# Performance work log

Hardware: AMD Instinct MI355X
Metric: run time of the kernel (lower is better)

## Reference

```python
import jax, jax.numpy as jnp
import numpy as np

D_IN = 384
HID = 384
D_OUT = 384

def _kaiming(key, fan_in, fan_out):
    return jax.random.normal(key, (fan_in, fan_out), dtype=jnp.float32) * np.sqrt(2.0 / fan_in)

def setup_inputs() -> dict:
    key = jax.random.key(0)
    ks = jax.random.split(key, 12)
    B, O, T = 8, 1024, 8192
    obj_vecs = jax.random.normal(ks[0], (B, O, D_IN), dtype=jnp.float32)
    pred_vecs = jax.random.normal(ks[1], (B, T, D_IN), dtype=jnp.float32)
    edges = jax.random.randint(ks[2], (B, T, 2), 0, O, dtype=jnp.int64)
    # gconv1: [3D -> H -> 2H + Dout]; gconv2: [H -> H -> Dout]
    w1a = _kaiming(ks[3], 3 * D_IN, HID); b1a = jnp.zeros((HID,), jnp.float32)
    w1b = _kaiming(ks[4], HID, 2 * HID + D_OUT); b1b = jnp.zeros((2 * HID + D_OUT,), jnp.float32)
    w2a = _kaiming(ks[5], HID, HID); b2a = jnp.zeros((HID,), jnp.float32)
    w2b = _kaiming(ks[6], HID, D_OUT); b2b = jnp.zeros((D_OUT,), jnp.float32)
    return {"obj_vecs": obj_vecs, "pred_vecs": pred_vecs, "edges": edges,
            "w1a": w1a, "b1a": b1a, "w1b": w1b, "b1b": b1b,
            "w2a": w2a, "b2a": b2a, "w2b": w2b, "b2b": b2b}

def _gconv_forward(obj_vecs, pred_vecs, edges, w1a, b1a, w1b, b1b, w2a, b2a, w2b, b2b):
    B, O, D = obj_vecs.shape
    s_idx = edges[:, :, 0]  # (B, T)
    o_idx = edges[:, :, 1]
    batch = jnp.arange(B)[:, None]
    subj = obj_vecs[batch, s_idx]  # (B, T, D) gather
    objt = obj_vecs[batch, o_idx]
    triple = jnp.concatenate([subj, pred_vecs, objt], axis=-1)  # (B, T, 3D)
    h = jax.nn.relu(triple @ w1a + b1a)
    t = jax.nn.relu(h @ w1b + b1b)  # (B, T, 2H + Dout)
    new_s = t[:, :, :HID]
    new_p = t[:, :, HID:HID + D_OUT]
    new_o = t[:, :, HID + D_OUT:]
    # scatter_add per batch into (O, H) buffers
    def agg(si, oi, vs, vo):
        return jnp.zeros((O, HID), vs.dtype).at[si].add(vs).at[oi].add(vo)
    pooled = jax.vmap(agg)(s_idx, o_idx, new_s, new_o)  # (B, O, H)
    pooled = pooled / jnp.linalg.norm(pooled)  # global Frobenius norm, as in torch .norm()
    out_obj = jax.nn.relu(jax.nn.relu(pooled @ w2a + b2a) @ w2b + b2b)
    return out_obj, new_p

def reference(obj_vecs, pred_vecs, edges, w1a, b1a, w1b, b1b, w2a, b2a, w2b, b2b):
    return _gconv_forward(obj_vecs, pred_vecs, edges, w1a, b1a, w1b, b1b, w2a, b2a, w2b, b2b)
```

## Files before the change

### kernel.cpp

```cpp
#include <hip/hip_runtime.h>
#include <hip/hip_bf16.h>

#define NB 8
#define NT 8192
#define NO 1024
#define DD 384
#define K1 1152
#define M1 65536
#define MO 8192

typedef __attribute__((ext_vector_type(8))) short bf16x8;
typedef __attribute__((ext_vector_type(4))) float f32x4;
typedef __attribute__((ext_vector_type(4))) unsigned short u16x4;

__device__ __forceinline__ unsigned short f2bf(float f) {
    union { float f; unsigned u; } v; v.f = f;
    unsigned r = v.u + 0x7FFFu + ((v.u >> 16) & 1u);
    return (unsigned short)(r >> 16);
}
__device__ __forceinline__ float bf2f(unsigned short h) {
    union { unsigned u; float f; } v; v.u = ((unsigned)h) << 16;
    return v.f;
}
__device__ __forceinline__ bf16x8 pack8(f32x4 a, f32x4 b) {
    bf16x8 r;
    r[0] = (short)f2bf(a[0]); r[1] = (short)f2bf(a[1]);
    r[2] = (short)f2bf(a[2]); r[3] = (short)f2bf(a[3]);
    r[4] = (short)f2bf(b[0]); r[5] = (short)f2bf(b[1]);
    r[6] = (short)f2bf(b[2]); r[7] = (short)f2bf(b[3]);
    return r;
}
__device__ __forceinline__ void gload16(const void* g, void* l) {
    __builtin_amdgcn_global_load_lds(
        (const __attribute__((address_space(1))) unsigned int*)g,
        (__attribute__((address_space(3))) unsigned int*)l, 16, 0, 0);
}

__global__ void k_cvt4(const float* __restrict__ s, unsigned short* __restrict__ d, int n) {
    int i = (blockIdx.x * blockDim.x + threadIdx.x) * 4;
    if (i >= n) return;
    f32x4 v = *(const f32x4*)(s + i);
    u16x4 o;
    o[0] = f2bf(v[0]); o[1] = f2bf(v[1]); o[2] = f2bf(v[2]); o[3] = f2bf(v[3]);
    *(u16x4*)(d + i) = o;
}
__global__ void k_tr(const float* __restrict__ s, unsigned short* __restrict__ d, int K, int N) {
    int k = blockIdx.x;
    int n = blockIdx.y * blockDim.x + threadIdx.x;
    if (n < N) d[n * K + k] = f2bf(s[k * N + n]);
}

__global__ void k_ss1(const float* __restrict__ p, float* __restrict__ partial, int n4) {
    __shared__ float wsum[4];
    int stride = gridDim.x * blockDim.x;
    float s = 0.f;
    for (int i = blockIdx.x * blockDim.x + threadIdx.x; i < n4; i += stride) {
        f32x4 v = *(const f32x4*)(p + i * 4);
        s += v[0] * v[0] + v[1] * v[1] + v[2] * v[2] + v[3] * v[3];
    }
#pragma unroll
    for (int off = 32; off; off >>= 1) s += __shfl_down(s, off, 64);
    if ((threadIdx.x & 63) == 0) wsum[threadIdx.x >> 6] = s;
    __syncthreads();
    if (threadIdx.x == 0)
        partial[blockIdx.x] = wsum[0] + wsum[1] + wsum[2] + wsum[3];
}
__global__ void k_ss2(const float* __restrict__ partial, float* __restrict__ o) {
    float s = partial[threadIdx.x];
#pragma unroll
    for (int off = 32; off; off >>= 1) s += __shfl_down(s, off, 64);
    __shared__ float w0, w1;
    if (threadIdx.x == 0) w0 = s;
    if (threadIdx.x == 64) w1 = s;
    __syncthreads();
    if (threadIdx.x == 0) o[0] = w0 + w1;
}
__global__ void k_normcvt(const float* __restrict__ p, const float* __restrict__ ss,
                          unsigned short* __restrict__ o) {
    int i = (blockIdx.x * blockDim.x + threadIdx.x) * 8;
    float s = rsqrtf(ss[0]);
    f32x4 a = *(const f32x4*)(p + i), b = *(const f32x4*)(p + i + 4);
    a *= s; b *= s;
    *(bf16x8*)(o + i) = pack8(a, b);
}

__global__ void k_hist(const int* __restrict__ edges, int* __restrict__ cnt) {
    int i = blockIdx.x * 256 + threadIdx.x;
    int2 e = *(const int2*)&edges[(size_t)i * 2];
    int b = i >> 13;
    atomicAdd(&cnt[(b << 10) + e.x], 1);
    atomicAdd(&cnt[(b << 10) + e.y], 1);
}
__global__ void k_scan(const int* __restrict__ cnt, int* __restrict__ offs) {
    __shared__ int a[1024];
    int b = blockIdx.x, t = threadIdx.x;
    int own = cnt[(b << 10) + t];
    a[t] = own;
    __syncthreads();
    for (int s = 1; s < 1024; s <<= 1) {
        int v = (t >= s) ? a[t - s] : 0;
        __syncthreads();
        a[t] += v;
        __syncthreads();
    }
    offs[(b << 10) + t] = a[t] - own;
}
__global__ void k_fill(const int* __restrict__ edges, const int* __restrict__ offs,
                       int* __restrict__ cur, int* __restrict__ elist) {
    int i = blockIdx.x * 256 + threadIdx.x;
    int2 e = *(const int2*)&edges[(size_t)i * 2];
    int b = i >> 13, t = i & (NT - 1);
    int ps = atomicAdd(&cur[(b << 10) + e.x], 1);
    elist[(b << 14) + offs[(b << 10) + e.x] + ps] = t * 2;
    int po = atomicAdd(&cur[(b << 10) + e.y], 1);
    elist[(b << 14) + offs[(b << 10) + e.y] + po] = t * 2 + 1;
}
__global__ void k_pool(const unsigned short* __restrict__ sob, const int* __restrict__ cnt,
                       const int* __restrict__ offs, const int* __restrict__ elist,
                       float* __restrict__ pooled) {
    int w = (blockIdx.x * 256 + threadIdx.x) >> 6;
    int lane = threadIdx.x & 63;
    if (lane >= 48) return;
    int b = w >> 10, o = w & (NO - 1);
    int len = cnt[(b << 10) + o];
    const int* lst = elist + (b << 14) + offs[(b << 10) + o];
    f32x4 a0 = {0.f, 0.f, 0.f, 0.f}, a1 = {0.f, 0.f, 0.f, 0.f};
    f32x4 c0 = {0.f, 0.f, 0.f, 0.f}, c1 = {0.f, 0.f, 0.f, 0.f};
    int j = 0;
    for (; j + 1 < len; j += 2) {
        int e0 = lst[j], e1 = lst[j + 1];
        bf16x8 v0 = *(const bf16x8*)(sob + ((size_t)((b << 13) + (e0 >> 1))) * 768 + (e0 & 1) * DD + lane * 8);
        bf16x8 v1 = *(const bf16x8*)(sob + ((size_t)((b << 13) + (e1 >> 1))) * 768 + (e1 & 1) * DD + lane * 8);
        a0[0] += bf2f((unsigned short)v0[0]); a0[1] += bf2f((unsigned short)v0[1]);
        a0[2] += bf2f((unsigned short)v0[2]); a0[3] += bf2f((unsigned short)v0[3]);
        a1[0] += bf2f((unsigned short)v0[4]); a1[1] += bf2f((unsigned short)v0[5]);
        a1[2] += bf2f((unsigned short)v0[6]); a1[3] += bf2f((unsigned short)v0[7]);
        c0[0] += bf2f((unsigned short)v1[0]); c0[1] += bf2f((unsigned short)v1[1]);
        c0[2] += bf2f((unsigned short)v1[2]); c0[3] += bf2f((unsigned short)v1[3]);
        c1[0] += bf2f((unsigned short)v1[4]); c1[1] += bf2f((unsigned short)v1[5]);
        c1[2] += bf2f((unsigned short)v1[6]); c1[3] += bf2f((unsigned short)v1[7]);
    }
    if (j < len) {
        int e0 = lst[j];
        bf16x8 v0 = *(const bf16x8*)(sob + ((size_t)((b << 13) + (e0 >> 1))) * 768 + (e0 & 1) * DD + lane * 8);
        a0[0] += bf2f((unsigned short)v0[0]); a0[1] += bf2f((unsigned short)v0[1]);
        a0[2] += bf2f((unsigned short)v0[2]); a0[3] += bf2f((unsigned short)v0[3]);
        a1[0] += bf2f((unsigned short)v0[4]); a1[1] += bf2f((unsigned short)v0[5]);
        a1[2] += bf2f((unsigned short)v0[6]); a1[3] += bf2f((unsigned short)v0[7]);
    }
    a0 += c0; a1 += c1;
    float* dst = pooled + ((size_t)((b << 10) + o)) * DD + lane * 8;
    *(f32x4*)dst = a0;
    *(f32x4*)(dst + 4) = a1;
}

template <int STAGE, int EPI>
__launch_bounds__(512, 2)
__global__ void gemm_k(const unsigned short* __restrict__ Abf,
                       const unsigned short* __restrict__ objb,
                       const float* __restrict__ predf,
                       const int* __restrict__ edges,
                       const unsigned short* __restrict__ Bt,
                       const float* __restrict__ bias,
                       unsigned short* __restrict__ outb,
                       float* __restrict__ outf,
                       int K, int ldC)
{
    const int tid = threadIdx.x;
    const int lane = tid & 63;
    const int m0 = blockIdx.x * 128;
    const int bt0 = 0;

    __shared__ unsigned short At[128 * 64];
    __shared__ unsigned short Bl[384 * 64];
    __shared__ int eidx[128][2];

    if (STAGE == 1) {
        if (tid < 128) {
            int2 e = *(const int2*)&edges[(size_t)(m0 + tid) * 2];
            eidx[tid][0] = e.x;
            eidx[tid][1] = e.y;
        }
        __syncthreads();
    }

    const int rb = tid >> 3;
    const int c8 = ((tid & 7) ^ (rb & 7)) * 8;

    int er0[2], er1[2];
    if (STAGE == 1) {
        const int bb = (m0 >> 13) << 10;
#pragma unroll
        for (int i = 0; i < 2; ++i) {
            er0[i] = bb + eidx[i * 64 + rb][0];
            er1[i] = bb + eidx[i * 64 + rb][1];
        }
    }

    f32x4 acc[4][6];
#pragma unroll
    for (int i = 0; i < 4; ++i)
#pragma unroll
        for (int j = 0; j < 6; ++j) acc[i][j] = (f32x4){0.f, 0.f, 0.f, 0.f};

    const int wid = tid >> 6, wm = wid >> 2, wn = wid & 3;
    const int l16 = lane & 15, lg = lane >> 4;

    for (int kk = 0; kk < K; kk += 64) {
#pragma unroll
        for (int i = 0; i < 6; ++i)
            gload16(Bt + (size_t)(bt0 + i * 64 + rb) * K + kk + c8, Bl + i * 4096 + tid * 8);
        if (STAGE == 0) {
#pragma unroll
            for (int i = 0; i < 2; ++i)
                gload16(Abf + (size_t)(m0 + i * 64 + rb) * K + kk + c8, At + i * 4096 + tid * 8);
        } else {
            const int seg = kk / DD;
            const int ko = kk - seg * DD;
            if (seg == 1) {
#pragma unroll
                for (int i = 0; i < 2; ++i) {
                    const float* p = predf + (size_t)(m0 + i * 64 + rb) * DD + ko + c8;
                    *(bf16x8*)(At + i * 4096 + tid * 8) = pack8(*(const f32x4*)p, *(const f32x4*)(p + 4));
                }
            } else if (seg == 0) {
#pragma unroll
                for (int i = 0; i < 2; ++i)
                    gload16(objb + (size_t)er0[i] * DD + ko + c8, At + i * 4096 + tid * 8);
            } else {
#pragma unroll
                for (int i = 0; i < 2; ++i)
                    gload16(objb + (size_t)er1[i] * DD + ko + c8, At + i * 4096 + tid * 8);
            }
        }
        __syncthreads();
#pragma unroll
        for (int kt = 0; kt < 2; ++kt) {
            const int cs = ((kt * 4 + lg) ^ (l16 & 7)) * 8;
            bf16x8 af[4], bfr[6];
#pragma unroll
            for (int mt = 0; mt < 4; ++mt)
                af[mt] = *(const bf16x8*)(At + (wm * 64 + mt * 16 + l16) * 64 + cs);
#pragma unroll
            for (int nt = 0; nt < 6; ++nt)
                bfr[nt] = *(const bf16x8*)(Bl + (wn * 96 + nt * 16 + l16) * 64 + cs);
#pragma unroll
            for (int mt = 0; mt < 4; ++mt)
#pragma unroll
                for (int nt = 0; nt < 6; ++nt)
                    acc[mt][nt] = __builtin_amdgcn_mfma_f32_16x16x32_bf16(af[mt], bfr[nt], acc[mt][nt], 0, 0, 0);
        }
        __syncthreads();
    }

#pragma unroll
    for (int nt = 0; nt < 6; ++nt) {
        int gn = wn * 96 + nt * 16 + l16;
        float bv = bias[bt0 + gn];
#pragma unroll
        for (int mt = 0; mt < 4; ++mt) {
            int rbase = wm * 64 + mt * 16 + lg * 4;
#pragma unroll
            for (int rg = 0; rg < 4; ++rg) {
                int gr = m0 + rbase + rg;
                float v = fmaxf(acc[mt][nt][rg] + bv, 0.0f);
                if (EPI == 0) outb[(size_t)gr * ldC + gn] = f2bf(v);
                else          outf[(size_t)gr * ldC + gn] = v;
            }
        }
    }
}

template <int EPI>
__launch_bounds__(512, 1)
__global__ void gemm_p(const unsigned short* __restrict__ Abf,
                       const unsigned short* __restrict__ Bt,
                       const float* __restrict__ bias,
                       unsigned short* __restrict__ outb,
                       float* __restrict__ outf,
                       int K, int ldC, int bt0p, int btys, int cstride)
{
    const int tid = threadIdx.x;
    const int lane = tid & 63;
    const int m0 = blockIdx.x * 128;
    const int bt0 = bt0p + (int)blockIdx.y * btys;
    const int col0 = (int)blockIdx.y * cstride;

    __shared__ unsigned short lds[2][32768];

    const int rb = tid >> 3;
    const int c8 = ((tid & 7) ^ (rb & 7)) * 8;

    f32x4 acc[4][6];
#pragma unroll
    for (int i = 0; i < 4; ++i)
#pragma unroll
        for (int j = 0; j < 6; ++j) acc[i][j] = (f32x4){0.f, 0.f, 0.f, 0.f};

    const int wid = tid >> 6, wm = wid >> 2, wn = wid & 3;
    const int l16 = lane & 15, lg = lane >> 4;

#define STAGE_P(BUF, KK)                                                                   \
    {                                                                                      \
        _Pragma("unroll")                                                                  \
        for (int i = 0; i < 6; ++i)                                                        \
            gload16(Bt + (size_t)(bt0 + i * 64 + rb) * K + (KK) + c8,                      \
                    &lds[BUF][8192 + i * 4096 + tid * 8]);                                 \
        _Pragma("unroll")                                                                  \
        for (int i = 0; i < 2; ++i)                                                        \
            gload16(Abf + (size_t)(m0 + i * 64 + rb) * K + (KK) + c8,                      \
                    &lds[BUF][i * 4096 + tid * 8]);                                        \
    }

    const int nt = K / 64;
    STAGE_P(0, 0)
    for (int t = 0; t < nt; ++t) {
        const int cur = t & 1;
        if (t + 1 < nt) {
            STAGE_P(cur ^ 1, (t + 1) * 64)
            asm volatile("s_waitcnt vmcnt(8)" ::: "memory");
        } else {
            asm volatile("s_waitcnt vmcnt(0)" ::: "memory");
        }
        __builtin_amdgcn_s_barrier();
        const unsigned short* At = &lds[cur][0];
        const unsigned short* Bl = &lds[cur][8192];
#pragma unroll
        for (int kt = 0; kt < 2; ++kt) {
            const int cs = ((kt * 4 + lg) ^ (l16 & 7)) * 8;
            bf16x8 af[4], bfr[6];
#pragma unroll
            for (int mt = 0; mt < 4; ++mt)
                af[mt] = *(const bf16x8*)(At + (wm * 64 + mt * 16 + l16) * 64 + cs);
#pragma unroll
            for (int nn = 0; nn < 6; ++nn)
                bfr[nn] = *(const bf16x8*)(Bl + (wn * 96 + nn * 16 + l16) * 64 + cs);
#pragma unroll
            for (int mt = 0; mt < 4; ++mt)
#pragma unroll
                for (int nn = 0; nn < 6; ++nn)
                    acc[mt][nn] = __builtin_amdgcn_mfma_f32_16x16x32_bf16(af[mt], bfr[nn], acc[mt][nn], 0, 0, 0);
        }
        asm volatile("s_waitcnt lgkmcnt(0)" ::: "memory");
        __builtin_amdgcn_s_barrier();
    }
#undef STAGE_P

#pragma unroll
    for (int nn = 0; nn < 6; ++nn) {
        int gn = wn * 96 + nn * 16 + l16;
        float bv = bias[bt0 + gn];
#pragma unroll
        for (int mt = 0; mt < 4; ++mt) {
            int rbase = wm * 64 + mt * 16 + lg * 4;
#pragma unroll
            for (int rg = 0; rg < 4; ++rg) {
                int gr = m0 + rbase + rg;
                float v = fmaxf(acc[mt][nn][rg] + bv, 0.0f);
                if (EPI == 0) outb[(size_t)gr * ldC + col0 + gn] = f2bf(v);
                else          outf[(size_t)gr * ldC + col0 + gn] = v;
            }
        }
    }
}

extern "C" void kernel_launch(void* const* d_in, const int* in_sizes, int n_in,
                              void* d_out, int out_size, void* d_ws, size_t ws_size,
                              hipStream_t stream)
{
    const float* obj  = (const float*)d_in[0];
    const float* pred = (const float*)d_in[1];
    const int* edges  = (const int*)d_in[2];
    const float* w1a  = (const float*)d_in[3];
    const float* b1a  = (const float*)d_in[4];
    const float* w1b  = (const float*)d_in[5];
    const float* b1b  = (const float*)d_in[6];
    const float* w2a  = (const float*)d_in[7];
    const float* b2a  = (const float*)d_in[8];
    const float* w2b  = (const float*)d_in[9];
    const float* b2b  = (const float*)d_in[10];

    float* out_obj = (float*)d_out;
    float* newp    = out_obj + (size_t)MO * DD;
    unsigned short* sob = (unsigned short*)newp;

    unsigned short* objb = (unsigned short*)d_ws;
    unsigned short* w1aT = objb + (size_t)NB * NO * DD;
    unsigned short* w1bT = w1aT + (size_t)DD * K1;
    unsigned short* w2aT = w1bT + (size_t)K1 * DD;
    unsigned short* w2bT = w2aT + (size_t)DD * DD;
    unsigned short* hbuf = w2bT + (size_t)DD * DD;
    float* pooled = (float*)(hbuf + (size_t)M1 * DD);
    float* sumsq  = pooled + (size_t)MO * DD;
    unsigned short* hid2 = (unsigned short*)(sumsq + 4);
    int* cnt   = (int*)(hid2 + (size_t)MO * DD);
    int* cur   = cnt + NB * NO;
    int* offs  = cur + NB * NO;
    int* elist = offs + NB * NO;
    float* partial = (float*)(elist + 2 * M1);
    unsigned short* poolb = objb;

    hipLaunchKernelGGL(k_cvt4, dim3(3072), dim3(256), 0, stream, obj, objb, NB * NO * DD);
    hipLaunchKernelGGL(k_tr, dim3(K1, 3), dim3(128), 0, stream, w1a, w1aT, K1, DD);
    hipLaunchKernelGGL(k_tr, dim3(DD, 9), dim3(128), 0, stream, w1b, w1bT, DD, K1);
    hipLaunchKernelGGL(k_tr, dim3(DD, 3), dim3(128), 0, stream, w2a, w2aT, DD, DD);
    hipLaunchKernelGGL(k_tr, dim3(DD, 3), dim3(128), 0, stream, w2b, w2bT, DD, DD);
    hipMemsetAsync(cnt, 0, 2 * NB * NO * sizeof(int), stream);

    hipLaunchKernelGGL((gemm_k<1, 0>), dim3(M1 / 128, 1), dim3(512), 0, stream,
                       (const unsigned short*)nullptr, objb, pred, edges,
                       w1aT, b1a, hbuf, (float*)nullptr, K1, DD);

    hipLaunchKernelGGL((gemm_p<0>), dim3(M1 / 128, 2), dim3(512), 0, stream,
                       hbuf, w1bT, b1b, sob, (float*)nullptr, DD, 2 * DD, 0, 2 * DD, DD);

    hipLaunchKernelGGL(k_hist, dim3(256), dim3(256), 0, stream, edges, cnt);
    hipLaunchKernelGGL(k_scan, dim3(8), dim3(1024), 0, stream, cnt, offs);
    hipLaunchKernelGGL(k_fill, dim3(256), dim3(256), 0, stream, edges, offs, cur, elist);
    hipLaunchKernelGGL(k_pool, dim3(2048), dim3(256), 0, stream, sob, cnt, offs, elist, pooled);

    hipLaunchKernelGGL((gemm_p<2>), dim3(M1 / 128, 1), dim3(512), 0, stream,
                       hbuf, w1bT, b1b, (unsigned short*)nullptr, newp, DD, DD, DD, 0, 0);

    hipLaunchKernelGGL(k_ss1, dim3(128), dim3(256), 0, stream, pooled, partial, MO * DD / 4);
    hipLaunchKernelGGL(k_ss2, dim3(1), dim3(128), 0, stream, partial, sumsq);
    hipLaunchKernelGGL(k_normcvt, dim3(1536), dim3(256), 0, stream, pooled, sumsq, poolb);

    hipLaunchKernelGGL((gemm_p<0>), dim3(MO / 128, 1), dim3(512), 0, stream,
                       poolb, w2aT, b2a, hid2, (float*)nullptr, DD, DD, 0, 0, 0);

    hipLaunchKernelGGL((gemm_p<2>), dim3(MO / 128, 1), dim3(512), 0, stream,
                       hid2, w2bT, b2b, (unsigned short*)nullptr, out_obj, DD, DD, 0, 0, 0);
}
```

Baseline: 284.5 us.

## Double-buffer LDS in first gather GEMM to overlap loads with MFMA

Replaces the templated gemm_k with a dedicated gemm_g1 kernel for the first layer. It double-buffers the A and B tiles in shared memory (128 KB total) and prefetches the next K-step's gathered object rows, converted pred rows and weight tiles while MFMAs run on the current buffer. Waits use explicit vmcnt counts with raw barriers. The larger LDS footprint drops occupancy to one block per CU, which trades latency hiding from extra blocks for in-block overlap. pack8 gains some redundant duplicate assignments that have no effect.

```diff
diff --git a/kernel.cpp b/kernel.cpp
--- a/kernel.cpp
+++ b/kernel.cpp
@@ -27,7 +27,9 @@
     r[0] = (short)f2bf(a[0]); r[1] = (short)f2bf(a[1]);
     r[2] = (short)f2bf(a[2]); r[3] = (short)f2bf(a[3]);
     r[4] = (short)f2bf(b[0]); r[5] = (short)f2bf(b[1]);
-    r[6] = (short)f2bf(b[2]); r[7] = (short)f2bf(b[3]);
+    r[6] = (short)f2bf(b[2]); r[7] = (short)f2bf(b[7-4]);
+    r[7] = (short)f2bf(b[3]);
+    r[6] = (short)f2bf(b[2]);
     return r;
 }
 __device__ __forceinline__ void gload16(const void* g, void* l) {
@@ -154,47 +156,30 @@
     *(f32x4*)(dst + 4) = a1;
 }
 
-template <int STAGE, int EPI>
-__launch_bounds__(512, 2)
-__global__ void gemm_k(const unsigned short* __restrict__ Abf,
-                       const unsigned short* __restrict__ objb,
-                       const float* __restrict__ predf,
-                       const int* __restrict__ edges,
-                       const unsigned short* __restrict__ Bt,
-                       const float* __restrict__ bias,
-                       unsigned short* __restrict__ outb,
-                       float* __restrict__ outf,
-                       int K, int ldC)
+__launch_bounds__(512, 1)
+__global__ void gemm_g1(const unsigned short* __restrict__ objb,
+                        const float* __restrict__ predf,
+                        const int* __restrict__ edges,
+                        const unsigned short* __restrict__ Bt,
+                        const float* __restrict__ bias,
+                        unsigned short* __restrict__ outb)
 {
     const int tid = threadIdx.x;
     const int lane = tid & 63;
     const int m0 = blockIdx.x * 128;
-    const int bt0 = 0;
-
-    __shared__ unsigned short At[128 * 64];
-    __shared__ unsigned short Bl[384 * 64];
-    __shared__ int eidx[128][2];
-
-    if (STAGE == 1) {
-        if (tid < 128) {
-            int2 e = *(const int2*)&edges[(size_t)(m0 + tid) * 2];
-            eidx[tid][0] = e.x;
-            eidx[tid][1] = e.y;
-        }
-        __syncthreads();
-    }
+
+    __shared__ unsigned short lds[2][32768];
 
     const int rb = tid >> 3;
     const int c8 = ((tid & 7) ^ (rb & 7)) * 8;
 
+    const int bb = (m0 >> 13) << 10;
     int er0[2], er1[2];
-    if (STAGE == 1) {
-        const int bb = (m0 >> 13) << 10;
-#pragma unroll
-        for (int i = 0; i < 2; ++i) {
-            er0[i] = bb + eidx[i * 64 + rb][0];
-            er1[i] = bb + eidx[i * 64 + rb][1];
-        }
+#pragma unroll
+    for (int i = 0; i < 2; ++i) {
+        int2 e = *(const int2*)&edges[(size_t)(m0 + i * 64 + rb) * 2];
+        er0[i] = bb + e.x;
+        er1[i] = bb + e.y;
     }
 
     f32x4 acc[4][6];
@@ -206,34 +191,54 @@
     const int wid = tid >> 6, wm = wid >> 2, wn = wid & 3;
     const int l16 = lane & 15, lg = lane >> 4;
 
-    for (int kk = 0; kk < K; kk += 64) {
-#pragma unroll
-        for (int i = 0; i < 6; ++i)
-            gload16(Bt + (size_t)(bt0 + i * 64 + rb) * K + kk + c8, Bl + i * 4096 + tid * 8);
-        if (STAGE == 0) {
-#pragma unroll
-            for (int i = 0; i < 2; ++i)
-                gload16(Abf + (size_t)(m0 + i * 64 + rb) * K + kk + c8, At + i * 4096 + tid * 8);
-        } else {
-            const int seg = kk / DD;
-            const int ko = kk - seg * DD;
-            if (seg == 1) {
+#pragma unroll
+    for (int i = 0; i < 2; ++i)
+        gload16(objb + (size_t)er0[i] * DD + c8, &lds[0][i * 4096 + tid * 8]);
+#pragma unroll
+    for (int i = 0; i < 6; ++i)
+        gload16(Bt + (size_t)(i * 64 + rb) * K1 + c8, &lds[0][8192 + i * 4096 + tid * 8]);
+
+    const int nsteps = K1 / 64;
+    for (int t = 0; t < nsteps; ++t) {
+        const int cur = t & 1;
+        const int tn = t + 1;
+        if (tn < nsteps) {
+            const int nseg = tn / 6;
+            const int ko = (tn - nseg * 6) * 64;
+            if (nseg == 1) {
+                f32x4 pf[2][2];
 #pragma unroll
                 for (int i = 0; i < 2; ++i) {
                     const float* p = predf + (size_t)(m0 + i * 64 + rb) * DD + ko + c8;
-                    *(bf16x8*)(At + i * 4096 + tid * 8) = pack8(*(const f32x4*)p, *(const f32x4*)(p + 4));
+                    pf[i][0] = *(const f32x4*)p;
+                    pf[i][1] = *(const f32x4*)(p + 4);
                 }
-            } else if (seg == 0) {
+#pragma unroll
+                for (int i = 0; i < 6; ++i)
+                    gload16(Bt + (size_t)(i * 64 + rb) * K1 + tn * 64 + c8,
+                            &lds[cur ^ 1][8192 + i * 4096 + tid * 8]);
 #pragma unroll
                 for (int i = 0; i < 2; ++i)
-                    gload16(objb + (size_t)er0[i] * DD + ko + c8, At + i * 4096 + tid * 8);
+                    *(bf16x8*)(&lds[cur ^ 1][i * 4096 + tid * 8]) = pack8(pf[i][0], pf[i][1]);
             } else {
-#pragma unroll
-                for (int i = 0; i < 2; ++i)
-                    gload16(objb + (size_t)er1[i] * DD + ko + c8, At + i * 4096 + tid * 8);
+                const unsigned short* asrc0 = (nseg == 0) ? objb + (size_t)er0[0] * DD + ko + c8
+                                                          : objb + (size_t)er1[0] * DD + ko + c8;
+                const unsigned short* asrc1 = (nseg == 0) ? objb + (size_t)er0[1] * DD + ko + c8
+                                                          : objb + (size_t)er1[1] * DD + ko + c8;
+                gload16(asrc0, &lds[cur ^ 1][0 * 4096 + tid * 8]);
+                gload16(asrc1, &lds[cur ^ 1][1 * 4096 + tid * 8]);
+#pragma unroll
+                for (int i = 0; i < 6; ++i)
+                    gload16(Bt + (size_t)(i * 64 + rb) * K1 + tn * 64 + c8,
+                            &lds[cur ^ 1][8192 + i * 4096 + tid * 8]);
+                asm volatile("s_waitcnt vmcnt(8)" ::: "memory");
             }
-        }
-        __syncthreads();
+        } else {
+            asm volatile("s_waitcnt vmcnt(0)" ::: "memory");
+        }
+        __builtin_amdgcn_s_barrier();
+        const unsigned short* At = &lds[cur][0];
+        const unsigned short* Bl = &lds[cur][8192];
 #pragma unroll
         for (int kt = 0; kt < 2; ++kt) {
             const int cs = ((kt * 4 + lg) ^ (l16 & 7)) * 8;
@@ -242,30 +247,30 @@
             for (int mt = 0; mt < 4; ++mt)
                 af[mt] = *(const bf16x8*)(At + (wm * 64 + mt * 16 + l16) * 64 + cs);
 #pragma unroll
-            for (int nt = 0; nt < 6; ++nt)
-                bfr[nt] = *(const bf16x8*)(Bl + (wn * 96 + nt * 16 + l16) * 64 + cs);
+            for (int nn = 0; nn < 6; ++nn)
+                bfr[nn] = *(const bf16x8*)(Bl + (wn * 96 + nn * 16 + l16) * 64 + cs);
 #pragma unroll
             for (int mt = 0; mt < 4; ++mt)
 #pragma unroll
-                for (int nt = 0; nt < 6; ++nt)
-                    acc[mt][nt] = __builtin_amdgcn_mfma_f32_16x16x32_bf16(af[mt], bfr[nt], acc[mt][nt], 0, 0, 0);
-        }
-        __syncthreads();
-    }
-
-#pragma unroll
-    for (int nt = 0; nt < 6; ++nt) {
-        int gn = wn * 96 + nt * 16 + l16;
-        float bv = bias[bt0 + gn];
+                for (int nn = 0; nn < 6; ++nn)
+                    acc[mt][nn] = __builtin_amdgcn_mfma_f32_16x16x32_bf16(af[mt], bfr[nn], acc[mt][nn], 0, 0, 0);
+        }
+        asm volatile("s_waitcnt lgkmcnt(0)" ::: "memory");
+        __builtin_amdgcn_s_barrier();
+    }
+
+#pragma unroll
+    for (int nn = 0; nn < 6; ++nn) {
+        int gn = wn * 96 + nn * 16 + l16;
+        float bv = bias[gn];
 #pragma unroll
         for (int mt = 0; mt < 4; ++mt) {
             int rbase = wm * 64 + mt * 16 + lg * 4;
 #pragma unroll
             for (int rg = 0; rg < 4; ++rg) {
                 int gr = m0 + rbase + rg;
-                float v = fmaxf(acc[mt][nt][rg] + bv, 0.0f);
-                if (EPI == 0) outb[(size_t)gr * ldC + gn] = f2bf(v);
-                else          outf[(size_t)gr * ldC + gn] = v;
+                float v = fmaxf(acc[mt][nn][rg] + bv, 0.0f);
+                outb[(size_t)gr * DD + gn] = f2bf(v);
             }
         }
     }
@@ -407,9 +412,8 @@
     hipLaunchKernelGGL(k_tr, dim3(DD, 3), dim3(128), 0, stream, w2b, w2bT, DD, DD);
     hipMemsetAsync(cnt, 0, 2 * NB * NO * sizeof(int), stream);
 
-    hipLaunchKernelGGL((gemm_k<1, 0>), dim3(M1 / 128, 1), dim3(512), 0, stream,
-                       (const unsigned short*)nullptr, objb, pred, edges,
-                       w1aT, b1a, hbuf, (float*)nullptr, K1, DD);
+    hipLaunchKernelGGL(gemm_g1, dim3(M1 / 128), dim3(512), 0, stream,
+                       objb, pred, edges, w1aT, b1a, hbuf);
 
     hipLaunchKernelGGL((gemm_p<0>), dim3(M1 / 128, 2), dim3(512), 0, stream,
                        hbuf, w1bT, b1b, sob, (float*)nullptr, DD, 2 * DD, 0, 2 * DD, DD);
```

After: 274.4 us. 1.04x faster.
